# Kernel optimization log

Measured on AMD Instinct MI355X. Metric: run time of the kernel, lower is better.

The kernel has to match this reference:

```python
import jax, jax.numpy as jnp
import numpy as np

B = 1024          # number of graphs
H = 8             # heads
EPS = 1e-5        # LayerNorm eps (torch default)
MEAN_RES_SCALE = 0.2


def _ln(x, w, b):
    mu = x.mean(-1, keepdims=True)
    var = ((x - mu) ** 2).mean(-1, keepdims=True)
    return (x - mu) / jnp.sqrt(var + EPS) * w + b


def setup_inputs() -> dict:
    key = jax.random.key(0)
    ks = jax.random.split(key, 10)
    N, D = 262144, 256
    s = 1.0 / np.sqrt(D)
    return {
        "h": jax.random.normal(ks[0], (N, D), jnp.float32),
        "batch": jnp.sort(jax.random.randint(ks[1], (N,), 0, B)),
        "cdr_mask": jax.random.bernoulli(ks[2], 0.2, (N,)),
        "iface_mask": jax.random.bernoulli(ks[3], 0.2, (N,)),
        "ln_kv_w": jnp.ones((D,), jnp.float32),
        "ln_kv_b": jnp.zeros((D,), jnp.float32),
        "ln_q_w": jnp.ones((D,), jnp.float32),
        "ln_q_b": jnp.zeros((D,), jnp.float32),
        "Wk": jax.random.normal(ks[4], (D, D), jnp.float32) * s,
        "Wv": jax.random.normal(ks[5], (D, D), jnp.float32) * s,
        "Wq": jax.random.normal(ks[6], (D, 2 * D), jnp.float32) * (1.0 / np.sqrt(2 * D)),
        "Wres": jax.random.normal(ks[7], (D, D), jnp.float32) * s,
        "Wout": jax.random.normal(ks[8], (D, D), jnp.float32) * s,
        "cdr_bias": jnp.asarray(0.6, jnp.float32),
        "iface_bias": jnp.asarray(0.8, jnp.float32),
        "logit_scale": jnp.asarray(1.0, jnp.float32),
    }


def reference(h, batch, cdr_mask, iface_mask, ln_kv_w, ln_kv_b, ln_q_w, ln_q_b,
              Wk, Wv, Wq, Wres, Wout, cdr_bias, iface_bias, logit_scale):
    N, D = h.shape
    hd = D // H
    # per-graph mean / max pooling (segment reductions; all segments non-empty)
    counts = jax.ops.segment_sum(jnp.ones((N,), h.dtype), batch, num_segments=B)[:, None]
    mean_raw = jax.ops.segment_sum(h, batch, num_segments=B) / counts      # [B,D]
    max_raw = jax.ops.segment_max(h, batch, num_segments=B)                # [B,D]
    # single query per graph (dropout = identity in eval)
    q = jnp.concatenate([mean_raw, max_raw], axis=-1) @ Wq.T               # [B,D]
    q = _ln(q, ln_q_w, ln_q_b).reshape(B, H, hd)                           # [B,H,hd]
    # keys / values per node
    h_ln = _ln(h, ln_kv_w, ln_kv_b)
    k = (h_ln @ Wk.T).reshape(N, H, hd)
    v = (h_ln @ Wv.T).reshape(N, H, hd)
    # attention logits with mask biases
    logit = (k * q[batch]).sum(-1) * (logit_scale / np.sqrt(hd))           # [N,H]
    logit = logit + cdr_bias * cdr_mask.astype(h.dtype)[:, None]
    logit = logit + iface_bias * iface_mask.astype(h.dtype)[:, None]
    # segment softmax over nodes of each graph
    m = jax.ops.segment_max(logit, batch, num_segments=B)                  # [B,H]
    e = jnp.exp(logit - m[batch])
    z = jax.ops.segment_sum(e, batch, num_segments=B)                      # [B,H]
    attn = e / z[batch]                                                    # [N,H]
    g = jax.ops.segment_sum(attn[..., None] * v, batch, num_segments=B)    # [B,H,hd]
    g = g.reshape(B, D)
    return g @ Wout.T + MEAN_RES_SCALE * (mean_raw @ Wres.T)               # [B,D]
```

## Files before the change

### kernel.cpp

```cpp
#include <hip/hip_runtime.h>

__global__ void k_offsets(const int* __restrict__ batch, const int* __restrict__ cdr,
                          const int* __restrict__ ifm, const float* __restrict__ cdr_bias,
                          const float* __restrict__ iface_bias,
                          int* __restrict__ start, float* __restrict__ mbias,
                          int N, int B) {
    int i = blockIdx.x * blockDim.x + threadIdx.x;
    if (i >= N) return;
    mbias[i] = cdr_bias[0] * (float)cdr[i] + iface_bias[0] * (float)ifm[i];
    int b = batch[i];
    if (i == 0) {
        for (int g = 0; g <= b; ++g) start[g] = 0;
    } else {
        int pb = batch[i - 1];
        for (int g = pb + 1; g <= b; ++g) start[g] = i;
    }
    if (i == N - 1) {
        for (int g = b + 1; g <= B; ++g) start[g] = N;
    }
}

#define STAT_CAP 768

__global__ __launch_bounds__(256) void k_fused(
    const float* __restrict__ h, const int* __restrict__ start,
    const float* __restrict__ mbias,
    const float* __restrict__ lnkw, const float* __restrict__ lnkb,
    const float* __restrict__ Wq, const float* __restrict__ Wk,
    const float* __restrict__ ln_q_w, const float* __restrict__ ln_q_b,
    const float* __restrict__ logit_scale,
    const float* __restrict__ Wv, const float* __restrict__ Wout,
    const float* __restrict__ Wres,
    float* __restrict__ out)
{
    const int g = blockIdx.x;
    const int tid = threadIdx.x;
    const int w = tid >> 6;
    const int l = tid & 63;
    const int hh = l >> 3;
    const int p = l & 7;
    const int s = start[g], e = start[g + 1];
    const int len = e - s;

    __shared__ __align__(16) float SMEM[8448];
    __shared__ __align__(16) float hbuf[4][288];
    __shared__ __align__(16) float MR[256];
    __shared__ float MW[4][8], ZW[4][8], SW[4][8], FG[4][8], IZ[8], SG[8];
    __shared__ float rs[4], rq[4];

    float* const PS  = SMEM;
    float* const PM  = SMEM + 1024;
    float* const X   = SMEM;
    float* const QL  = SMEM + 512;
    float* const WE  = SMEM + 768;
    float* const STT = SMEM + 2880;

    {
        float4 sm = make_float4(0.f, 0.f, 0.f, 0.f);
        float4 mx = make_float4(-INFINITY, -INFINITY, -INFINITY, -INFINITY);

        #define PROC(v, rowidx) do { \
            sm.x += (v).x; sm.y += (v).y; sm.z += (v).z; sm.w += (v).w; \
            mx.x = fmaxf(mx.x, (v).x); mx.y = fmaxf(mx.y, (v).y); \
            mx.z = fmaxf(mx.z, (v).z); mx.w = fmaxf(mx.w, (v).w); \
            float s1_ = ((v).x + (v).y) + ((v).z + (v).w); \
            float s2_ = fmaf((v).x, (v).x, fmaf((v).y, (v).y, fmaf((v).z, (v).z, (v).w * (v).w))); \
            s1_ += __shfl_xor(s1_, 1);  s2_ += __shfl_xor(s2_, 1); \
            s1_ += __shfl_xor(s1_, 2);  s2_ += __shfl_xor(s2_, 2); \
            s1_ += __shfl_xor(s1_, 4);  s2_ += __shfl_xor(s2_, 4); \
            s1_ += __shfl_xor(s1_, 8);  s2_ += __shfl_xor(s2_, 8); \
            s1_ += __shfl_xor(s1_, 16); s2_ += __shfl_xor(s2_, 16); \
            s1_ += __shfl_xor(s1_, 32); s2_ += __shfl_xor(s2_, 32); \
            const int ri_ = (rowidx) - s; \
            if (l == 0 && ri_ < STAT_CAP) { \
                const float mu_ = s1_ * (1.f / 256.f); \
                const float var_ = s2_ * (1.f / 256.f) - mu_ * mu_; \
                *(float2*)(&STT[2 * ri_]) = make_float2(mu_, rsqrtf(var_ + 1e-5f)); \
            } } while (0)

        int n = s + w;
        if (n + 12 < e) {
            float4 f0 = *(const float4*)(h + (size_t)(n)      * 256 + l * 4);
            float4 f1 = *(const float4*)(h + (size_t)(n + 4)  * 256 + l * 4);
            float4 f2 = *(const float4*)(h + (size_t)(n + 8)  * 256 + l * 4);
            float4 f3 = *(const float4*)(h + (size_t)(n + 12) * 256 + l * 4);
            for (; n + 28 < e; n += 16) {
                PROC(f0, n);      f0 = *(const float4*)(h + (size_t)(n + 16) * 256 + l * 4);
                PROC(f1, n + 4);  f1 = *(const float4*)(h + (size_t)(n + 20) * 256 + l * 4);
                PROC(f2, n + 8);  f2 = *(const float4*)(h + (size_t)(n + 24) * 256 + l * 4);
                PROC(f3, n + 12); f3 = *(const float4*)(h + (size_t)(n + 28) * 256 + l * 4);
            }
            PROC(f0, n); PROC(f1, n + 4); PROC(f2, n + 8); PROC(f3, n + 12);
            n += 16;
        }
        for (; n < e; n += 4) {
            const float4 a = *(const float4*)(h + (size_t)n * 256 + l * 4);
            PROC(a, n);
        }
        #undef PROC

        *(float4*)(&PS[w * 256 + l * 4]) = sm;
        *(float4*)(&PM[w * 256 + l * 4]) = mx;
    }
    __syncthreads();

    const int d = tid;
    {
        const float sum = (PS[d] + PS[256 + d]) + (PS[512 + d] + PS[768 + d]);
        const float mxv = fmaxf(fmaxf(PM[d], PM[256 + d]),
                                fmaxf(PM[512 + d], PM[768 + d]));
        const float mean = sum / (float)len;
        MR[d] = mean;
        X[d] = mean;
        X[256 + d] = mxv;
    }
    __syncthreads();

    {
        float q = 0.f;
        const float* wqr = Wq + (size_t)d * 512;
        #pragma unroll 8
        for (int j = 0; j < 512; j += 4) {
            float4 w4 = *(const float4*)(wqr + j);
            q += w4.x * X[j] + w4.y * X[j + 1] + w4.z * X[j + 2] + w4.w * X[j + 3];
        }
        float s1 = q, s2 = q * q;
        #pragma unroll
        for (int off = 1; off < 64; off <<= 1) {
            s1 += __shfl_xor(s1, off);
            s2 += __shfl_xor(s2, off);
        }
        if ((d & 63) == 0) { rs[d >> 6] = s1; rq[d >> 6] = s2; }
        __syncthreads();
        const float t1 = rs[0] + rs[1] + rs[2] + rs[3];
        const float t2 = rq[0] + rq[1] + rq[2] + rq[3];
        const float mu = t1 * (1.f / 256.f);
        const float var = t2 * (1.f / 256.f) - mu * mu;
        const float rstd = rsqrtf(var + 1e-5f);
        QL[d] = (q - mu) * rstd * ln_q_w[d] + ln_q_b[d];
        __syncthreads();

        const float scale = logit_scale[0] * 0.17677669529663687f;
        const float fold = scale * lnkw[d];
        #pragma unroll
        for (int h2 = 0; h2 < 8; ++h2) {
            float a = 0.f;
            #pragma unroll 8
            for (int r = 0; r < 32; ++r) {
                a += Wk[(size_t)(h2 * 32 + r) * 256 + d] * QL[h2 * 32 + r];
            }
            WE[h2 * 264 + d] = a * fold;
        }
    }
    __syncthreads();

    float we[32];
    #pragma unroll
    for (int r = 0; r < 8; ++r) {
        float4 t = *(const float4*)(&WE[hh * 264 + p * 32 + r * 4]);
        we[4 * r + 0] = t.x; we[4 * r + 1] = t.y; we[4 * r + 2] = t.z; we[4 * r + 3] = t.w;
    }
    float s1h = 0.f;
    #pragma unroll
    for (int r = 0; r < 32; ++r) s1h += we[r];
    s1h += __shfl_xor(s1h, 1);
    s1h += __shfl_xor(s1h, 2);
    s1h += __shfl_xor(s1h, 4);

    float m = -INFINITY, z = 0.f, sw = 0.f;
    float u[32];
    #pragma unroll
    for (int r = 0; r < 32; ++r) u[r] = 0.f;

    const int wofs = l * 4 + ((l >> 3) << 2);
    const int rofs = p * 36;

    {
        int n = s + w;
        float4 x0 = make_float4(0.f, 0.f, 0.f, 0.f);
        float4 x1 = x0;
        float b0 = 0.f, b1 = 0.f;
        if (n < e)     { x0 = *(const float4*)(h + (size_t)n * 256 + l * 4);       b0 = mbias[n]; }
        if (n + 4 < e) { x1 = *(const float4*)(h + (size_t)(n + 4) * 256 + l * 4); b1 = mbias[n + 4]; }

        while (n < e) {
            const float4 xc = x0;
            const float bc = b0;
            x0 = x1; b0 = b1;
            if (n + 8 < e) {
                x1 = *(const float4*)(h + (size_t)(n + 8) * 256 + l * 4);
                b1 = mbias[n + 8];
            }

            float mu, rstd;
            const int ri = n - s;
            if (ri < STAT_CAP) {
                const float2 tc = *(const float2*)(&STT[2 * ri]);
                mu = tc.x; rstd = tc.y;
            } else {
                float s1 = (xc.x + xc.y) + (xc.z + xc.w);
                float s2 = fmaf(xc.x, xc.x, fmaf(xc.y, xc.y, fmaf(xc.z, xc.z, xc.w * xc.w)));
                #pragma unroll
                for (int off = 1; off < 64; off <<= 1) {
                    s1 += __shfl_xor(s1, off);
                    s2 += __shfl_xor(s2, off);
                }
                mu = s1 * (1.f / 256.f);
                rstd = rsqrtf(s2 * (1.f / 256.f) - mu * mu + 1e-5f);
            }

            *(float4*)(&hbuf[w][wofs]) = xc;
            asm volatile("s_waitcnt lgkmcnt(0)" ::: "memory");

            float hv[32];
            #pragma unroll
            for (int r = 0; r < 8; ++r) {
                float4 t = *(const float4*)(&hbuf[w][rofs + r * 4]);
                hv[4 * r + 0] = t.x; hv[4 * r + 1] = t.y; hv[4 * r + 2] = t.z; hv[4 * r + 3] = t.w;
            }
            float d0 = 0.f, d1 = 0.f, d2 = 0.f, d3 = 0.f;
            #pragma unroll
            for (int r = 0; r < 8; ++r) {
                d0 = fmaf(hv[4 * r + 0], we[4 * r + 0], d0);
                d1 = fmaf(hv[4 * r + 1], we[4 * r + 1], d1);
                d2 = fmaf(hv[4 * r + 2], we[4 * r + 2], d2);
                d3 = fmaf(hv[4 * r + 3], we[4 * r + 3], d3);
            }
            float dt = (d0 + d1) + (d2 + d3);
            dt += __shfl_xor(dt, 1);
            dt += __shfl_xor(dt, 2);
            dt += __shfl_xor(dt, 4);

            const float lv = fmaf(rstd, dt - mu * s1h, bc);
            const float nm = fmaxf(m, lv);
            const float ee = __expf(lv - nm);
            const float c = ee * rstd;
            if (__any(lv > m)) {
                const float a = __expf(m - nm);
                z = z * a + ee;
                sw = sw * a + c * mu;
                #pragma unroll
                for (int r = 0; r < 32; ++r) u[r] = u[r] * a + c * hv[r];
                m = nm;
            } else {
                z += ee;
                sw += c * mu;
                #pragma unroll
                for (int r = 0; r < 32; ++r) u[r] = fmaf(c, hv[r], u[r]);
            }
            n += 4;
        }
    }

    __syncthreads();
    if (p == 0) { MW[w][hh] = m; ZW[w][hh] = z; SW[w][hh] = sw; }
    #pragma unroll
    for (int r = 0; r < 8; ++r) {
        float4 t = make_float4(u[4 * r], u[4 * r + 1], u[4 * r + 2], u[4 * r + 3]);
        *(float4*)(&SMEM[w * 2112 + hh * 264 + p * 32 + r * 4]) = t;
    }
    __syncthreads();

    if (tid < 8) {
        const float mg = fmaxf(fmaxf(MW[0][tid], MW[1][tid]),
                               fmaxf(MW[2][tid], MW[3][tid]));
        float zg = 0.f, sg = 0.f;
        #pragma unroll
        for (int ww = 0; ww < 4; ++ww) {
            const float f = __expf(MW[ww][tid] - mg);
            FG[ww][tid] = f;
            zg += ZW[ww][tid] * f;
            sg += SW[ww][tid] * f;
        }
        IZ[tid] = 1.f / zg;
        SG[tid] = sg;
    }
    __syncthreads();

    float un[8];
    {
        const float lwj = lnkw[tid], lbj = lnkb[tid];
        #pragma unroll
        for (int h2 = 0; h2 < 8; ++h2) {
            const float Uv = SMEM[0 * 2112 + h2 * 264 + tid] * FG[0][h2]
                           + SMEM[1 * 2112 + h2 * 264 + tid] * FG[1][h2]
                           + SMEM[2 * 2112 + h2 * 264 + tid] * FG[2][h2]
                           + SMEM[3 * 2112 + h2 * 264 + tid] * FG[3][h2];
            un[h2] = (Uv - SG[h2]) * IZ[h2] * lwj + lbj;
        }
    }
    __syncthreads();
    #pragma unroll
    for (int h2 = 0; h2 < 8; ++h2) SMEM[h2 * 256 + tid] = un[h2];
    __syncthreads();

    {
        const int h5 = d >> 5;
        float acc = 0.f;
        const float* wvr = Wv + (size_t)d * 256;
        #pragma unroll 8
        for (int j = 0; j < 256; j += 4) {
            const float4 wv = *(const float4*)(wvr + j);
            const float4 uv = *(const float4*)(&SMEM[h5 * 256 + j]);
            acc += wv.x * uv.x + wv.y * uv.y + wv.z * uv.z + wv.w * uv.w;
        }
        SMEM[2048 + d] = acc;
    }
    __syncthreads();
    {
        float oo = 0.f, rr = 0.f;
        const float* wor = Wout + (size_t)d * 256;
        const float* wrr = Wres + (size_t)d * 256;
        #pragma unroll 8
        for (int j = 0; j < 256; j += 4) {
            const float4 wo = *(const float4*)(wor + j);
            const float4 wq = *(const float4*)(wrr + j);
            const float4 gf = *(const float4*)(&SMEM[2048 + j]);
            const float4 mr = *(const float4*)(&MR[j]);
            oo += wo.x * gf.x + wo.y * gf.y + wo.z * gf.z + wo.w * gf.w;
            rr += wq.x * mr.x + wq.y * mr.y + wq.z * mr.z + wq.w * mr.w;
        }
        out[(size_t)g * 256 + d] = oo + 0.2f * rr;
    }
}

extern "C" void kernel_launch(void* const* d_in, const int* in_sizes, int n_in,
                              void* d_out, int out_size, void* d_ws, size_t ws_size,
                              hipStream_t stream)
{
    const float* h        = (const float*)d_in[0];
    const int*   batch    = (const int*)d_in[1];
    const int*   cdr      = (const int*)d_in[2];
    const int*   ifm      = (const int*)d_in[3];
    const float* ln_kv_w  = (const float*)d_in[4];
    const float* ln_kv_b  = (const float*)d_in[5];
    const float* ln_q_w   = (const float*)d_in[6];
    const float* ln_q_b   = (const float*)d_in[7];
    const float* Wk       = (const float*)d_in[8];
    const float* Wv       = (const float*)d_in[9];
    const float* Wq       = (const float*)d_in[10];
    const float* Wres     = (const float*)d_in[11];
    const float* Wout     = (const float*)d_in[12];
    const float* cdr_b    = (const float*)d_in[13];
    const float* if_b     = (const float*)d_in[14];
    const float* lsc      = (const float*)d_in[15];

    const int N = in_sizes[0] / 256;
    const int B = out_size / 256;

    int*   start = (int*)d_ws;
    float* mbias = (float*)((char*)d_ws + 8192);

    k_offsets<<<(N + 255) / 256, 256, 0, stream>>>(batch, cdr, ifm, cdr_b, if_b,
                                                   start, mbias, N, B);
    k_fused<<<B, 256, 0, stream>>>(h, start, mbias, ln_kv_w, ln_kv_b,
                                   Wq, Wk, ln_q_w, ln_q_b, lsc,
                                   Wv, Wout, Wres, (float*)d_out);
}
```

Baseline: 619.7 us.

## Process two rows per wave iteration in attention loop and reuse shared memory

Each wave now handles two node rows per iteration (rows n and n+1, stride 8) instead of one, so the shuffle reductions, max/exp rescale and loop overhead are amortized over two rows. Prefetch depth doubles to four float4 loads in flight per lane. The per-wave row staging buffers move into the existing SMEM region, which requires an extra block barrier, and the loop re-reads staged rows from LDS instead of holding them in registers. This trades register pressure for more LDS traffic and more outstanding loads.

```diff
diff --git a/kernel.cpp b/kernel.cpp
--- a/kernel.cpp
+++ b/kernel.cpp
@@ -43,7 +43,6 @@
     const int len = e - s;
 
     __shared__ __align__(16) float SMEM[8448];
-    __shared__ __align__(16) float hbuf[4][288];
     __shared__ __align__(16) float MR[256];
     __shared__ float MW[4][8], ZW[4][8], SW[4][8], FG[4][8], IZ[8], SG[8];
     __shared__ float rs[4], rq[4];
@@ -54,6 +53,7 @@
     float* const QL  = SMEM + 512;
     float* const WE  = SMEM + 768;
     float* const STT = SMEM + 2880;
+    float* const HB  = SMEM;
 
     {
         float4 sm = make_float4(0.f, 0.f, 0.f, 0.f);
@@ -166,6 +166,7 @@
     s1h += __shfl_xor(s1h, 1);
     s1h += __shfl_xor(s1h, 2);
     s1h += __shfl_xor(s1h, 4);
+    __syncthreads();
 
     float m = -INFINITY, z = 0.f, sw = 0.f;
     float u[32];
@@ -174,81 +175,110 @@
 
     const int wofs = l * 4 + ((l >> 3) << 2);
     const int rofs = p * 36;
-
-    {
-        int n = s + w;
-        float4 x0 = make_float4(0.f, 0.f, 0.f, 0.f);
-        float4 x1 = x0;
-        float b0 = 0.f, b1 = 0.f;
-        if (n < e)     { x0 = *(const float4*)(h + (size_t)n * 256 + l * 4);       b0 = mbias[n]; }
-        if (n + 4 < e) { x1 = *(const float4*)(h + (size_t)(n + 4) * 256 + l * 4); b1 = mbias[n + 4]; }
+    float* const rowA = HB + w * 576;
+    float* const rowB = HB + w * 576 + 288;
+
+    {
+        int n = s + 2 * w;
+        float4 xa0 = make_float4(0.f, 0.f, 0.f, 0.f), xb0 = xa0, xa1 = xa0, xb1 = xa0;
+        float ba0 = 0.f, bb0 = 0.f, ba1 = 0.f, bb1 = 0.f;
+        if (n < e)     { xa0 = *(const float4*)(h + (size_t)n * 256 + l * 4);       ba0 = mbias[n]; }
+        if (n + 1 < e) { xb0 = *(const float4*)(h + (size_t)(n + 1) * 256 + l * 4); bb0 = mbias[n + 1]; }
+        if (n + 8 < e) { xa1 = *(const float4*)(h + (size_t)(n + 8) * 256 + l * 4); ba1 = mbias[n + 8]; }
+        if (n + 9 < e) { xb1 = *(const float4*)(h + (size_t)(n + 9) * 256 + l * 4); bb1 = mbias[n + 9]; }
 
         while (n < e) {
-            const float4 xc = x0;
-            const float bc = b0;
-            x0 = x1; b0 = b1;
-            if (n + 8 < e) {
-                x1 = *(const float4*)(h + (size_t)(n + 8) * 256 + l * 4);
-                b1 = mbias[n + 8];
-            }
-
-            float mu, rstd;
-            const int ri = n - s;
-            if (ri < STAT_CAP) {
-                const float2 tc = *(const float2*)(&STT[2 * ri]);
-                mu = tc.x; rstd = tc.y;
+            const float4 xA = xa0, xB = xb0;
+            const float bA = ba0, bB = bb0;
+            xa0 = xa1; xb0 = xb1; ba0 = ba1; bb0 = bb1;
+            if (n + 16 < e) { xa1 = *(const float4*)(h + (size_t)(n + 16) * 256 + l * 4); ba1 = mbias[n + 16]; }
+            if (n + 17 < e) { xb1 = *(const float4*)(h + (size_t)(n + 17) * 256 + l * 4); bb1 = mbias[n + 17]; }
+
+            const int ri0 = n - s;
+            const bool hasB = (n + 1 < e);
+            float muA, rsA, muB, rsB;
+            if (ri0 < STAT_CAP) {
+                const float2 t = *(const float2*)(&STT[2 * ri0]);
+                muA = t.x; rsA = t.y;
             } else {
-                float s1 = (xc.x + xc.y) + (xc.z + xc.w);
-                float s2 = fmaf(xc.x, xc.x, fmaf(xc.y, xc.y, fmaf(xc.z, xc.z, xc.w * xc.w)));
+                float s1 = (xA.x + xA.y) + (xA.z + xA.w);
+                float s2 = fmaf(xA.x, xA.x, fmaf(xA.y, xA.y, fmaf(xA.z, xA.z, xA.w * xA.w)));
                 #pragma unroll
-                for (int off = 1; off < 64; off <<= 1) {
-                    s1 += __shfl_xor(s1, off);
-                    s2 += __shfl_xor(s2, off);
+                for (int off = 1; off < 64; off <<= 1) { s1 += __shfl_xor(s1, off); s2 += __shfl_xor(s2, off); }
+                muA = s1 * (1.f / 256.f);
+                rsA = rsqrtf(s2 * (1.f / 256.f) - muA * muA + 1e-5f);
+            }
+            if (hasB) {
+                if (ri0 + 1 < STAT_CAP) {
+                    const float2 t = *(const float2*)(&STT[2 * ri0 + 2]);
+                    muB = t.x; rsB = t.y;
+                } else {
+                    float s1 = (xB.x + xB.y) + (xB.z + xB.w);
+                    float s2 = fmaf(xB.x, xB.x, fmaf(xB.y, xB.y, fmaf(xB.z, xB.z, xB.w * xB.w)));
+                    #pragma unroll
+                    for (int off = 1; off < 64; off <<= 1) { s1 += __shfl_xor(s1, off); s2 += __shfl_xor(s2, off); }
+                    muB = s1 * (1.f / 256.f);
+                    rsB = rsqrtf(s2 * (1.f / 256.f) - muB * muB + 1e-5f);
                 }
-                mu = s1 * (1.f / 256.f);
-                rstd = rsqrtf(s2 * (1.f / 256.f) - mu * mu + 1e-5f);
-            }
-
-            *(float4*)(&hbuf[w][wofs]) = xc;
+            } else { muB = 0.f; rsB = 0.f; }
+
+            *(float4*)(rowA + wofs) = xA;
+            *(float4*)(rowB + wofs) = xB;
             asm volatile("s_waitcnt lgkmcnt(0)" ::: "memory");
 
-            float hv[32];
+            float dA0 = 0.f, dA1 = 0.f, dA2 = 0.f, dA3 = 0.f;
+            float dB0 = 0.f, dB1 = 0.f, dB2 = 0.f, dB3 = 0.f;
             #pragma unroll
             for (int r = 0; r < 8; ++r) {
-                float4 t = *(const float4*)(&hbuf[w][rofs + r * 4]);
-                hv[4 * r + 0] = t.x; hv[4 * r + 1] = t.y; hv[4 * r + 2] = t.z; hv[4 * r + 3] = t.w;
-            }
-            float d0 = 0.f, d1 = 0.f, d2 = 0.f, d3 = 0.f;
-            #pragma unroll
-            for (int r = 0; r < 8; ++r) {
-                d0 = fmaf(hv[4 * r + 0], we[4 * r + 0], d0);
-                d1 = fmaf(hv[4 * r + 1], we[4 * r + 1], d1);
-                d2 = fmaf(hv[4 * r + 2], we[4 * r + 2], d2);
-                d3 = fmaf(hv[4 * r + 3], we[4 * r + 3], d3);
-            }
-            float dt = (d0 + d1) + (d2 + d3);
-            dt += __shfl_xor(dt, 1);
-            dt += __shfl_xor(dt, 2);
-            dt += __shfl_xor(dt, 4);
-
-            const float lv = fmaf(rstd, dt - mu * s1h, bc);
-            const float nm = fmaxf(m, lv);
-            const float ee = __expf(lv - nm);
-            const float c = ee * rstd;
-            if (__any(lv > m)) {
+                const float4 ta = *(const float4*)(rowA + rofs + r * 4);
+                const float4 tb = *(const float4*)(rowB + rofs + r * 4);
+                dA0 = fmaf(ta.x, we[4 * r + 0], dA0); dA1 = fmaf(ta.y, we[4 * r + 1], dA1);
+                dA2 = fmaf(ta.z, we[4 * r + 2], dA2); dA3 = fmaf(ta.w, we[4 * r + 3], dA3);
+                dB0 = fmaf(tb.x, we[4 * r + 0], dB0); dB1 = fmaf(tb.y, we[4 * r + 1], dB1);
+                dB2 = fmaf(tb.z, we[4 * r + 2], dB2); dB3 = fmaf(tb.w, we[4 * r + 3], dB3);
+            }
+            float dtA = (dA0 + dA1) + (dA2 + dA3);
+            float dtB = (dB0 + dB1) + (dB2 + dB3);
+            dtA += __shfl_xor(dtA, 1); dtB += __shfl_xor(dtB, 1);
+            dtA += __shfl_xor(dtA, 2); dtB += __shfl_xor(dtB, 2);
+            dtA += __shfl_xor(dtA, 4); dtB += __shfl_xor(dtB, 4);
+
+            const float lvA = fmaf(rsA, dtA - muA * s1h, bA);
+            const float lvB = hasB ? fmaf(rsB, dtB - muB * s1h, bB) : -INFINITY;
+
+            const float nm = fmaxf(m, fmaxf(lvA, lvB));
+            const float eA = __expf(lvA - nm);
+            const float eB = __expf(lvB - nm);
+            const float cA = eA * rsA;
+            const float cB = eB * rsB;
+            if (__any(nm > m)) {
                 const float a = __expf(m - nm);
-                z = z * a + ee;
-                sw = sw * a + c * mu;
+                z = z * a + (eA + eB);
+                sw = sw * a + (cA * muA + cB * muB);
                 #pragma unroll
-                for (int r = 0; r < 32; ++r) u[r] = u[r] * a + c * hv[r];
+                for (int r = 0; r < 8; ++r) {
+                    const float4 ta = *(const float4*)(rowA + rofs + r * 4);
+                    const float4 tb = *(const float4*)(rowB + rofs + r * 4);
+                    u[4 * r + 0] = fmaf(u[4 * r + 0], a, fmaf(cA, ta.x, cB * tb.x));
+                    u[4 * r + 1] = fmaf(u[4 * r + 1], a, fmaf(cA, ta.y, cB * tb.y));
+                    u[4 * r + 2] = fmaf(u[4 * r + 2], a, fmaf(cA, ta.z, cB * tb.z));
+                    u[4 * r + 3] = fmaf(u[4 * r + 3], a, fmaf(cA, ta.w, cB * tb.w));
+                }
                 m = nm;
             } else {
-                z += ee;
-                sw += c * mu;
+                z += eA + eB;
+                sw += cA * muA + cB * muB;
                 #pragma unroll
-                for (int r = 0; r < 32; ++r) u[r] = fmaf(c, hv[r], u[r]);
-            }
-            n += 4;
+                for (int r = 0; r < 8; ++r) {
+                    const float4 ta = *(const float4*)(rowA + rofs + r * 4);
+                    const float4 tb = *(const float4*)(rowB + rofs + r * 4);
+                    u[4 * r + 0] = fmaf(cA, ta.x, fmaf(cB, tb.x, u[4 * r + 0]));
+                    u[4 * r + 1] = fmaf(cA, ta.y, fmaf(cB, tb.y, u[4 * r + 1]));
+                    u[4 * r + 2] = fmaf(cA, ta.z, fmaf(cB, tb.z, u[4 * r + 2]));
+                    u[4 * r + 3] = fmaf(cA, ta.w, fmaf(cB, tb.w, u[4 * r + 3]));
+                }
+            }
+            n += 8;
         }
     }
 
```

Measured after the change: 611.3 us. Within noise of the previous version (-1.4%).
